# Kernel tuning notes

Measured on AMD Instinct MI355X. Metric: run time of the kernel, lower is better.

The kernel has to match this reference:

```python
import jax, jax.numpy as jnp
import numpy as np

EMBED_DIM = 128
NUM_HEADS = 16
D_K = EMBED_DIM // NUM_HEADS  # 8 qubits per head
DEPTH = 2

# Sign matrix for PauliZ expectations: wire w corresponds to bit (D_K-1-w) of the
# flattened state index (wire 0 = most significant axis, torchquantum convention).
_idx = np.arange(2 ** D_K)
_SIGNS = np.stack([1.0 - 2.0 * ((_idx >> (D_K - 1 - w)) & 1) for w in range(D_K)], axis=1).astype(np.float32)  # [2^d_k, d_k]


def quantum_layer(tokens, qparams):
    """Simulate the variational circuit for a batch of tokens.
    tokens: [N, d_k] real angles; qparams: [depth, d_k] trainable RX angles.
    RX(a)RX(b)=RX(a+b) on the same wire, so encoder + all depth RX layers
    compose into a single RX per wire. Then `depth` CNOT ladders, then <Z_w>.
    """
    theta = tokens + jnp.sum(qparams, axis=0)  # [N, d_k]
    half = 0.5 * theta
    # single-qubit amplitudes after RX(theta)|0>: [cos(t/2), -i sin(t/2)]
    amp = jnp.stack([jnp.cos(half).astype(jnp.complex64),
                     (-1j) * jnp.sin(half).astype(jnp.complex64)], axis=-1)  # [N, d_k, 2]
    # build product state [N, 2, 2, ..., 2]
    state = amp[:, 0, :]
    for i in range(1, D_K):
        state = jnp.einsum('n...,nq->n...q', state, amp[:, i, :])
    # depth x CNOT ladder: CNOT(i, i+1) for i in 0..d_k-2
    for _ in range(DEPTH):
        for i in range(D_K - 1):
            c_ax = 1 + i
            c0 = jnp.take(state, 0, axis=c_ax)
            c1 = jnp.take(state, 1, axis=c_ax)
            c1 = jnp.flip(c1, axis=c_ax)  # target axis = c_ax+1, shifted by -1 after take
            state = jnp.stack([c0, c1], axis=c_ax)
    probs = (state.real ** 2 + state.imag ** 2).reshape(state.shape[0], -1)  # [N, 2^d_k]
    return probs @ jnp.asarray(_SIGNS)  # [N, d_k]


def setup_inputs() -> dict:
    key = jax.random.key(0)
    ks = jax.random.split(key, 6)
    B, S, E = 4, 512, EMBED_DIM
    scale = 1.0 / np.sqrt(E)
    return {
        'x': jax.random.normal(ks[0], (B, S, E), dtype=jnp.float32),
        'Wq': jax.random.normal(ks[1], (E, E), dtype=jnp.float32) * scale,
        'Wk': jax.random.normal(ks[2], (E, E), dtype=jnp.float32) * scale,
        'Wv': jax.random.normal(ks[3], (E, E), dtype=jnp.float32) * scale,
        'Wo': jax.random.normal(ks[4], (E, E), dtype=jnp.float32) * scale,
        'qparams': jax.random.normal(ks[5], (DEPTH, D_K), dtype=jnp.float32),
    }


def reference(x, Wq, Wk, Wv, Wo, qparams):
    B, S, E = x.shape
    H, dk = NUM_HEADS, D_K
    # linear projections (torch Linear, no bias): y = x @ W.T
    q = (x @ Wq.T).reshape(B, S, H, dk).transpose(0, 2, 1, 3)  # [B,H,S,dk]
    k = (x @ Wk.T).reshape(B, S, H, dk).transpose(0, 2, 1, 3)
    v = (x @ Wv.T).reshape(B, S, H, dk).transpose(0, 2, 1, 3)
    # batched quantum circuit over all (batch, head, seq) tokens; shared weights
    qq = quantum_layer(q.reshape(-1, dk), qparams).reshape(B, H, S, dk)
    kq = quantum_layer(k.reshape(-1, dk), qparams).reshape(B, H, S, dk)
    vq = quantum_layer(v.reshape(-1, dk), qparams).reshape(B, H, S, dk)
    scores = jnp.einsum('bhqd,bhkd->bhqk', qq, kq) / jnp.sqrt(jnp.float32(dk))
    attn = jax.nn.softmax(scores, axis=-1)  # dropout in eval mode: identity
    out = jnp.einsum('bhqk,bhkd->bhqd', attn, vq)
    out = out.transpose(0, 2, 1, 3).reshape(B, S, E)
    return out @ Wo.T
```

## Files before the change

kernel.cpp:

```cpp
#include <hip/hip_runtime.h>
#include <cmath>

#define MATSZ 262144
#define QKV_OFF 65536
#define AOUT_OFF (65536 + 3 * MATSZ)

__global__ __launch_bounds__(256, 3) void k_qkvq(
    const float* __restrict__ x, const float* __restrict__ Wq,
    const float* __restrict__ Wk, const float* __restrict__ Wv,
    const float* __restrict__ qp, float* __restrict__ ws) {
  __shared__ float xs[8][128];
  __shared__ float th[2][8][128];
  const int t = threadIdx.x;
  const int tile = blockIdx.x;
  const int m = blockIdx.y;
  const float* W = (m == 0) ? Wq : (m == 1) ? Wk : Wv;
  {
    ((float4*)&xs[0][0])[t] = ((const float4*)(x + (size_t)tile * 1024))[t];
  }
  const int e = t & 127, half = t >> 7;
  float4 w[16];
  {
    const float4* wr = (const float4*)W + (size_t)e * 32 + half * 16;
#pragma unroll
    for (int i = 0; i < 16; ++i) w[i] = wr[i];
  }
  __syncthreads();
  const float4* xs4 = (const float4*)&xs[0][0];
#pragma unroll
  for (int r = 0; r < 8; ++r) {
    float a = 0.f;
    const float4* xr = xs4 + r * 32 + half * 16;
#pragma unroll
    for (int i = 0; i < 16; ++i) {
      float4 xv = xr[i];
      a = fmaf(xv.x, w[i].x, a);
      a = fmaf(xv.y, w[i].y, a);
      a = fmaf(xv.z, w[i].z, a);
      a = fmaf(xv.w, w[i].w, a);
    }
    th[half][r][e] = a;
  }
  __syncthreads();
  const int cg = t & 31, rg = t >> 5;
  const float4* th4 = (const float4*)&th[0][0][0];
  float4 s0 = th4[rg * 32 + cg];
  float4 s1 = th4[256 + rg * 32 + cg];
  float4 a4 = make_float4(s0.x + s1.x, s0.y + s1.y, s0.z + s1.z, s0.w + s1.w);
  const int j0 = (cg & 1) * 4;
  float4 qs;
  qs.x = qp[j0 + 0] + qp[8 + j0 + 0];
  qs.y = qp[j0 + 1] + qp[8 + j0 + 1];
  qs.z = qp[j0 + 2] + qp[8 + j0 + 2];
  qs.w = qp[j0 + 3] + qp[8 + j0 + 3];
  float4 c;
  c.x = __cosf(a4.x + qs.x);
  c.y = __cosf(a4.y + qs.y);
  c.z = __cosf(a4.z + qs.z);
  c.w = __cosf(a4.w + qs.w);
  float4 u;
  u.x = c.x; u.y = c.y; u.z = c.x * c.z; u.w = c.y * c.w;
  float gz = __shfl_xor(u.z, 1);
  float gw = __shfl_xor(u.w, 1);
  const bool hi = (cg & 1) != 0;
  float mz = hi ? gz : 1.f, mw = hi ? gw : 1.f;
  float4 o;
  o.x = u.x * mz; o.y = u.y * mw; o.z = u.z * mz; o.w = u.w * mw;
  const int h = cg >> 1;
  int row = tile * 8 + rg;
  int b = row >> 9, s = row & 511;
  float* dst = ws + QKV_OFF + (size_t)m * MATSZ +
               ((size_t)((b << 4) + h) * 512 + s) * 8 + (hi ? 4 : 0);
  *(float4*)dst = o;
}

__global__ __launch_bounds__(256, 4) void k_attn(
    float* __restrict__ ws) {
  __shared__ float4 kslo[512], kshi[512], vslo[512], vshi[512];
  const int qt = blockIdx.x;
  const int bh = blockIdx.y;
  const float* qkv = ws + QKV_OFF;
  const float* Qg = qkv + (size_t)bh * 4096;
  const float4* Kg = (const float4*)(qkv + MATSZ + (size_t)bh * 4096);
  const float4* Vg = (const float4*)(qkv + 2 * (size_t)MATSZ + (size_t)bh * 4096);
  const int t = threadIdx.x;
  for (int k = t; k < 512; k += 256) {
    kslo[k] = Kg[2 * k]; kshi[k] = Kg[2 * k + 1];
    vslo[k] = Vg[2 * k]; vshi[k] = Vg[2 * k + 1];
  }
  __syncthreads();
  const int qslot = t >> 4, ko = t & 15;
  const int row0 = qt * 64 + qslot * 4;
  const float scale = 0.35355339059327373f;
  float4 qa[4], qb[4];
#pragma unroll
  for (int r = 0; r < 4; ++r) {
    qa[r] = ((const float4*)(Qg + (size_t)(row0 + r) * 8))[0];
    qb[r] = ((const float4*)(Qg + (size_t)(row0 + r) * 8))[1];
    qa[r].x *= scale; qa[r].y *= scale; qa[r].z *= scale; qa[r].w *= scale;
    qb[r].x *= scale; qb[r].y *= scale; qb[r].z *= scale; qb[r].w *= scale;
  }
  float l[4] = {0.f, 0.f, 0.f, 0.f};
  float a[4][8];
#pragma unroll
  for (int r = 0; r < 4; ++r)
#pragma unroll
    for (int j = 0; j < 8; ++j) a[r][j] = 0.f;
#pragma unroll 2
  for (int i = 0; i < 32; ++i) {
    int k = i * 16 + ko;
    float4 kx = kslo[k], ky = kshi[k];
    float4 vx = vslo[k], vy = vshi[k];
#pragma unroll
    for (int r = 0; r < 4; ++r) {
      float s = qa[r].x * kx.x + qa[r].y * kx.y + qa[r].z * kx.z + qa[r].w * kx.w +
                qb[r].x * ky.x + qb[r].y * ky.y + qb[r].z * ky.z + qb[r].w * ky.w;
      float p = __expf(s);
      l[r] += p;
      a[r][0] = fmaf(p, vx.x, a[r][0]);
      a[r][1] = fmaf(p, vx.y, a[r][1]);
      a[r][2] = fmaf(p, vx.z, a[r][2]);
      a[r][3] = fmaf(p, vx.w, a[r][3]);
      a[r][4] = fmaf(p, vy.x, a[r][4]);
      a[r][5] = fmaf(p, vy.y, a[r][5]);
      a[r][6] = fmaf(p, vy.z, a[r][6]);
      a[r][7] = fmaf(p, vy.w, a[r][7]);
    }
  }
#pragma unroll
  for (int mm = 1; mm <= 8; mm <<= 1) {
#pragma unroll
    for (int r = 0; r < 4; ++r) {
      l[r] += __shfl_xor(l[r], mm);
#pragma unroll
      for (int j = 0; j < 8; ++j) a[r][j] += __shfl_xor(a[r][j], mm);
    }
  }
  if (ko == 0) {
    int b = bh >> 4, h = bh & 15;
    float* aout = ws + AOUT_OFF;
#pragma unroll
    for (int r = 0; r < 4; ++r) {
      float inv = 1.f / l[r];
      float* d = aout + ((size_t)(b * 512 + row0 + r)) * 128 + h * 8;
      ((float4*)d)[0] = make_float4(a[r][0] * inv, a[r][1] * inv,
                                    a[r][2] * inv, a[r][3] * inv);
      ((float4*)d)[1] = make_float4(a[r][4] * inv, a[r][5] * inv,
                                    a[r][6] * inv, a[r][7] * inv);
    }
  }
}

__global__ __launch_bounds__(256, 3) void k_out(
    const float* __restrict__ ws, const float* __restrict__ Wo,
    float* __restrict__ out) {
  __shared__ float as_[8][128];
  __shared__ float th[2][8][128];
  const int t = threadIdx.x;
  const int tile = blockIdx.x;
  const float* aout = ws + AOUT_OFF;
  {
    ((float4*)&as_[0][0])[t] = ((const float4*)(aout + (size_t)tile * 1024))[t];
  }
  const int e = t & 127, half = t >> 7;
  float4 w[16];
  {
    const float4* wr = (const float4*)Wo + (size_t)e * 32 + half * 16;
#pragma unroll
    for (int i = 0; i < 16; ++i) w[i] = wr[i];
  }
  __syncthreads();
  const float4* as4 = (const float4*)&as_[0][0];
#pragma unroll
  for (int r = 0; r < 8; ++r) {
    float a = 0.f;
    const float4* ar = as4 + r * 32 + half * 16;
#pragma unroll
    for (int i = 0; i < 16; ++i) {
      float4 av = ar[i];
      a = fmaf(av.x, w[i].x, a);
      a = fmaf(av.y, w[i].y, a);
      a = fmaf(av.z, w[i].z, a);
      a = fmaf(av.w, w[i].w, a);
    }
    th[half][r][e] = a;
  }
  __syncthreads();
  const int cg = t & 31, rg = t >> 5;
  const float4* th4 = (const float4*)&th[0][0][0];
  float4 s0 = th4[rg * 32 + cg];
  float4 s1 = th4[256 + rg * 32 + cg];
  float4 o = make_float4(s0.x + s1.x, s0.y + s1.y, s0.z + s1.z, s0.w + s1.w);
  ((float4*)(out + (size_t)(tile * 8 + rg) * 128))[cg] = o;
}

extern "C" void kernel_launch(void* const* d_in, const int* in_sizes, int n_in,
                              void* d_out, int out_size, void* d_ws, size_t ws_size,
                              hipStream_t stream) {
  const float* x  = (const float*)d_in[0];
  const float* Wq = (const float*)d_in[1];
  const float* Wk = (const float*)d_in[2];
  const float* Wv = (const float*)d_in[3];
  const float* Wo = (const float*)d_in[4];
  const float* qp = (const float*)d_in[5];
  float* out = (float*)d_out;
  float* ws = (float*)d_ws;

  hipLaunchKernelGGL(k_qkvq, dim3(256, 3), dim3(256), 0, stream,
                     x, Wq, Wk, Wv, qp, ws);
  hipLaunchKernelGGL(k_attn, dim3(8, 64), dim3(256), 0, stream, ws);
  hipLaunchKernelGGL(k_out, dim3(256), dim3(256), 0, stream, ws, Wo, out);
}
```

Baseline: 41.61 us.

## Rework projection kernels to full-row per thread and restructure attention tiling

The projection kernels drop the split-K shared-memory reduction. Each of 128 threads now holds a full weight row and reads x straight from global memory. The quantum product is computed with wave shuffles, and the Q scale and log2(e) are folded into a constant so attention can use exp2f. Q is stored row-major, so attention reads it directly. Attention blocks handle 128 queries with 8 key lanes each, and the output projection uses 4-row tiles over 512 blocks. These changes remove shared-memory syncs and a separate scaling step, but double the per-thread weight register footprint and change occupancy.

```diff
diff --git a/kernel.cpp b/kernel.cpp
--- a/kernel.cpp
+++ b/kernel.cpp
@@ -2,104 +2,88 @@
 #include <cmath>
 
 #define MATSZ 262144
-#define QKV_OFF 65536
-#define AOUT_OFF (65536 + 3 * MATSZ)
 
-__global__ __launch_bounds__(256, 3) void k_qkvq(
+__global__ __launch_bounds__(128) void k_qkvq(
     const float* __restrict__ x, const float* __restrict__ Wq,
     const float* __restrict__ Wk, const float* __restrict__ Wv,
     const float* __restrict__ qp, float* __restrict__ ws) {
-  __shared__ float xs[8][128];
-  __shared__ float th[2][8][128];
-  const int t = threadIdx.x;
+  const int e = threadIdx.x;
   const int tile = blockIdx.x;
   const int m = blockIdx.y;
   const float* W = (m == 0) ? Wq : (m == 1) ? Wk : Wv;
+  float4 w[32];
   {
-    ((float4*)&xs[0][0])[t] = ((const float4*)(x + (size_t)tile * 1024))[t];
+    const float4* wr = (const float4*)W + (size_t)e * 32;
+#pragma unroll
+    for (int i = 0; i < 32; ++i) w[i] = wr[i];
   }
-  const int e = t & 127, half = t >> 7;
-  float4 w[16];
-  {
-    const float4* wr = (const float4*)W + (size_t)e * 32 + half * 16;
-#pragma unroll
-    for (int i = 0; i < 16; ++i) w[i] = wr[i];
-  }
-  __syncthreads();
-  const float4* xs4 = (const float4*)&xs[0][0];
+  float acc[8];
+  const float* xbase = x + (size_t)tile * 1024;
 #pragma unroll
   for (int r = 0; r < 8; ++r) {
+    const float4* xr = (const float4*)(xbase + r * 128);
     float a = 0.f;
-    const float4* xr = xs4 + r * 32 + half * 16;
 #pragma unroll
-    for (int i = 0; i < 16; ++i) {
+    for (int i = 0; i < 32; ++i) {
       float4 xv = xr[i];
       a = fmaf(xv.x, w[i].x, a);
       a = fmaf(xv.y, w[i].y, a);
       a = fmaf(xv.z, w[i].z, a);
       a = fmaf(xv.w, w[i].w, a);
     }
-    th[half][r][e] = a;
+    acc[r] = a;
   }
-  __syncthreads();
-  const int cg = t & 31, rg = t >> 5;
-  const float4* th4 = (const float4*)&th[0][0][0];
-  float4 s0 = th4[rg * 32 + cg];
-  float4 s1 = th4[256 + rg * 32 + cg];
-  float4 a4 = make_float4(s0.x + s1.x, s0.y + s1.y, s0.z + s1.z, s0.w + s1.w);
-  const int j0 = (cg & 1) * 4;
-  float4 qs;
-  qs.x = qp[j0 + 0] + qp[8 + j0 + 0];
-  qs.y = qp[j0 + 1] + qp[8 + j0 + 1];
-  qs.z = qp[j0 + 2] + qp[8 + j0 + 2];
-  qs.w = qp[j0 + 3] + qp[8 + j0 + 3];
-  float4 c;
-  c.x = __cosf(a4.x + qs.x);
-  c.y = __cosf(a4.y + qs.y);
-  c.z = __cosf(a4.z + qs.z);
-  c.w = __cosf(a4.w + qs.w);
-  float4 u;
-  u.x = c.x; u.y = c.y; u.z = c.x * c.z; u.w = c.y * c.w;
-  float gz = __shfl_xor(u.z, 1);
-  float gw = __shfl_xor(u.w, 1);
-  const bool hi = (cg & 1) != 0;
-  float mz = hi ? gz : 1.f, mw = hi ? gw : 1.f;
-  float4 o;
-  o.x = u.x * mz; o.y = u.y * mw; o.z = u.z * mz; o.w = u.w * mw;
-  const int h = cg >> 1;
-  int row = tile * 8 + rg;
-  int b = row >> 9, s = row & 511;
-  float* dst = ws + QKV_OFF + (size_t)m * MATSZ +
-               ((size_t)((b << 4) + h) * 512 + s) * 8 + (hi ? 4 : 0);
-  *(float4*)dst = o;
+  const int j = e & 7;
+  const int l = threadIdx.x & 63;
+  const float qs = qp[j] + qp[8 + j];
+  const float osc = (m == 0) ? 0.51013389376f : 1.0f;
+  const int h = e >> 3;
+  const int row0 = tile * 8;
+  const int b = row0 >> 9;
+#pragma unroll
+  for (int r = 0; r < 8; ++r) {
+    float c = __cosf(acc[r] + qs);
+    float t1 = __shfl(c, l - 2);
+    float x1 = (j >= 2) ? c * t1 : c;
+    float t2 = __shfl(x1, l - 4);
+    float x2 = (j >= 4) ? x1 * t2 : x1;
+    float o = x2 * osc;
+    int row = row0 + r;
+    if (m == 0) {
+      ws[(size_t)row * 128 + e] = o;
+    } else {
+      int s = row & 511;
+      ws[(size_t)m * MATSZ + ((size_t)((b << 4) + h) * 512 + s) * 8 + j] = o;
+    }
+  }
 }
 
-__global__ __launch_bounds__(256, 4) void k_attn(
-    float* __restrict__ ws) {
+__global__ __launch_bounds__(256) void k_attn(float* __restrict__ ws) {
   __shared__ float4 kslo[512], kshi[512], vslo[512], vshi[512];
   const int qt = blockIdx.x;
   const int bh = blockIdx.y;
-  const float* qkv = ws + QKV_OFF;
-  const float* Qg = qkv + (size_t)bh * 4096;
-  const float4* Kg = (const float4*)(qkv + MATSZ + (size_t)bh * 4096);
-  const float4* Vg = (const float4*)(qkv + 2 * (size_t)MATSZ + (size_t)bh * 4096);
+  const int b = bh >> 4, h = bh & 15;
+  const float* Kg = ws + MATSZ + (size_t)bh * 4096;
+  const float* Vg = ws + 2 * (size_t)MATSZ + (size_t)bh * 4096;
   const int t = threadIdx.x;
-  for (int k = t; k < 512; k += 256) {
-    kslo[k] = Kg[2 * k]; kshi[k] = Kg[2 * k + 1];
-    vslo[k] = Vg[2 * k]; vshi[k] = Vg[2 * k + 1];
+  {
+    const float4* Kg4 = (const float4*)Kg;
+    const float4* Vg4 = (const float4*)Vg;
+    for (int k = t; k < 512; k += 256) {
+      kslo[k] = Kg4[2 * k]; kshi[k] = Kg4[2 * k + 1];
+      vslo[k] = Vg4[2 * k]; vshi[k] = Vg4[2 * k + 1];
+    }
   }
-  __syncthreads();
-  const int qslot = t >> 4, ko = t & 15;
-  const int row0 = qt * 64 + qslot * 4;
-  const float scale = 0.35355339059327373f;
+  const int qslot = t >> 3, ko = t & 7;
+  const int srow0 = qt * 128 + qslot * 4;
   float4 qa[4], qb[4];
 #pragma unroll
   for (int r = 0; r < 4; ++r) {
-    qa[r] = ((const float4*)(Qg + (size_t)(row0 + r) * 8))[0];
-    qb[r] = ((const float4*)(Qg + (size_t)(row0 + r) * 8))[1];
-    qa[r].x *= scale; qa[r].y *= scale; qa[r].z *= scale; qa[r].w *= scale;
-    qb[r].x *= scale; qb[r].y *= scale; qb[r].z *= scale; qb[r].w *= scale;
+    const float* qrow = ws + ((size_t)(b * 512 + srow0 + r)) * 128 + h * 8;
+    qa[r] = ((const float4*)qrow)[0];
+    qb[r] = ((const float4*)qrow)[1];
   }
+  __syncthreads();
   float l[4] = {0.f, 0.f, 0.f, 0.f};
   float a[4][8];
 #pragma unroll
@@ -107,15 +91,16 @@
 #pragma unroll
     for (int j = 0; j < 8; ++j) a[r][j] = 0.f;
 #pragma unroll 2
-  for (int i = 0; i < 32; ++i) {
-    int k = i * 16 + ko;
+  for (int i = 0; i < 64; ++i) {
+    int k = i * 8 + ko;
     float4 kx = kslo[k], ky = kshi[k];
     float4 vx = vslo[k], vy = vshi[k];
 #pragma unroll
     for (int r = 0; r < 4; ++r) {
-      float s = qa[r].x * kx.x + qa[r].y * kx.y + qa[r].z * kx.z + qa[r].w * kx.w +
-                qb[r].x * ky.x + qb[r].y * ky.y + qb[r].z * ky.z + qb[r].w * ky.w;
-      float p = __expf(s);
+      float s = qa[r].x * kx.x + qa[r].y * kx.y + qa[r].z * kx.z +
+                qa[r].w * kx.w + qb[r].x * ky.x + qb[r].y * ky.y +
+                qb[r].z * ky.z + qb[r].w * ky.w;
+      float p = exp2f(s);
       l[r] += p;
       a[r][0] = fmaf(p, vx.x, a[r][0]);
       a[r][1] = fmaf(p, vx.y, a[r][1]);
@@ -128,7 +113,7 @@
     }
   }
 #pragma unroll
-  for (int mm = 1; mm <= 8; mm <<= 1) {
+  for (int mm = 1; mm <= 4; mm <<= 1) {
 #pragma unroll
     for (int r = 0; r < 4; ++r) {
       l[r] += __shfl_xor(l[r], mm);
@@ -137,12 +122,11 @@
     }
   }
   if (ko == 0) {
-    int b = bh >> 4, h = bh & 15;
-    float* aout = ws + AOUT_OFF;
+    float* aout = ws + 3 * (size_t)MATSZ;
 #pragma unroll
     for (int r = 0; r < 4; ++r) {
       float inv = 1.f / l[r];
-      float* d = aout + ((size_t)(b * 512 + row0 + r)) * 128 + h * 8;
+      float* d = aout + ((size_t)(b * 512 + srow0 + r)) * 128 + h * 8;
       ((float4*)d)[0] = make_float4(a[r][0] * inv, a[r][1] * inv,
                                     a[r][2] * inv, a[r][3] * inv);
       ((float4*)d)[1] = make_float4(a[r][4] * inv, a[r][5] * inv,
@@ -151,47 +135,32 @@
   }
 }
 
-__global__ __launch_bounds__(256, 3) void k_out(
+__global__ __launch_bounds__(128) void k_out(
     const float* __restrict__ ws, const float* __restrict__ Wo,
     float* __restrict__ out) {
-  __shared__ float as_[8][128];
-  __shared__ float th[2][8][128];
-  const int t = threadIdx.x;
+  const int e = threadIdx.x;
   const int tile = blockIdx.x;
-  const float* aout = ws + AOUT_OFF;
+  float4 w[32];
   {
-    ((float4*)&as_[0][0])[t] = ((const float4*)(aout + (size_t)tile * 1024))[t];
+    const float4* wr = (const float4*)Wo + (size_t)e * 32;
+#pragma unroll
+    for (int i = 0; i < 32; ++i) w[i] = wr[i];
   }
-  const int e = t & 127, half = t >> 7;
-  float4 w[16];
-  {
-    const float4* wr = (const float4*)Wo + (size_t)e * 32 + half * 16;
+  const float* aout = ws + 3 * (size_t)MATSZ + (size_t)tile * 512;
 #pragma unroll
-    for (int i = 0; i < 16; ++i) w[i] = wr[i];
-  }
-  __syncthreads();
-  const float4* as4 = (const float4*)&as_[0][0];
+  for (int r = 0; r < 4; ++r) {
+    const float4* ar = (const float4*)(aout + r * 128);
+    float a = 0.f;
 #pragma unroll
-  for (int r = 0; r < 8; ++r) {
-    float a = 0.f;
-    const float4* ar = as4 + r * 32 + half * 16;
-#pragma unroll
-    for (int i = 0; i < 16; ++i) {
+    for (int i = 0; i < 32; ++i) {
       float4 av = ar[i];
       a = fmaf(av.x, w[i].x, a);
       a = fmaf(av.y, w[i].y, a);
       a = fmaf(av.z, w[i].z, a);
       a = fmaf(av.w, w[i].w, a);
     }
-    th[half][r][e] = a;
+    out[(size_t)(tile * 4 + r) * 128 + e] = a;
   }
-  __syncthreads();
-  const int cg = t & 31, rg = t >> 5;
-  const float4* th4 = (const float4*)&th[0][0][0];
-  float4 s0 = th4[rg * 32 + cg];
-  float4 s1 = th4[256 + rg * 32 + cg];
-  float4 o = make_float4(s0.x + s1.x, s0.y + s1.y, s0.z + s1.z, s0.w + s1.w);
-  ((float4*)(out + (size_t)(tile * 8 + rg) * 128))[cg] = o;
 }
 
 extern "C" void kernel_launch(void* const* d_in, const int* in_sizes, int n_in,
@@ -206,8 +175,8 @@
   float* out = (float*)d_out;
   float* ws = (float*)d_ws;
 
-  hipLaunchKernelGGL(k_qkvq, dim3(256, 3), dim3(256), 0, stream,
+  hipLaunchKernelGGL(k_qkvq, dim3(256, 3), dim3(128), 0, stream,
                      x, Wq, Wk, Wv, qp, ws);
-  hipLaunchKernelGGL(k_attn, dim3(8, 64), dim3(256), 0, stream, ws);
-  hipLaunchKernelGGL(k_out, dim3(256), dim3(256), 0, stream, ws, Wo, out);
+  hipLaunchKernelGGL(k_attn, dim3(4, 64), dim3(256), 0, stream, ws);
+  hipLaunchKernelGGL(k_out, dim3(512), dim3(128), 0, stream, ws, Wo, out);
 }
```

Result: slower. 46.66 us (+12.2%).
